# Optimization experiments

Measured on AMD Instinct MI355X. Metric: run time of the kernel, lower is better.

Reference implementation:

```python
import jax, jax.numpy as jnp
import numpy as np

NN_SIZE = 10  # k nearest neighbors (includes the point itself)
EPS = 1e-8


def batch_normals(points_nchw, nn_size):
    # points_nchw: (B, 3, N)
    x = jnp.transpose(points_nchw, (0, 2, 1))  # (B, N, 3)
    sq = jnp.sum(x * x, axis=-1)  # (B, N)
    # pairwise squared distances (B, N, N)
    d2 = sq[:, :, None] + sq[:, None, :] - 2.0 * jnp.einsum('bnd,bmd->bnm', x, x)
    _, idx = jax.lax.top_k(-d2, nn_size)  # (B, N, k) nearest-neighbor indices
    # irregular gather of neighborhoods: (B, N, k, 3)
    neigh = jax.vmap(lambda p, i: p[i])(x, idx)
    centered = neigh - jnp.mean(neigh, axis=2, keepdims=True)
    # local 3x3 covariance per point
    cov = jnp.einsum('bnki,bnkj->bnij', centered, centered) / nn_size
    _, vecs = jnp.linalg.eigh(cov)  # eigenvalues ascending
    normals = vecs[..., 0]  # eigenvector of smallest eigenvalue, (B, N, 3), unit norm
    return jnp.transpose(normals, (0, 2, 1))  # (B, 3, N)


def setup_inputs() -> dict:
    key = jax.random.key(0)
    k1, k2 = jax.random.split(key)
    pred = jax.random.normal(k1, (8, 3, 4096), dtype=jnp.float32)
    gt = jax.random.normal(k2, (8, 3, 4096), dtype=jnp.float32)
    return {"pred": pred, "gt": gt}


def reference(pred, gt):
    pn = batch_normals(pred, NN_SIZE)  # (B, 3, N)
    gn = batch_normals(gt, NN_SIZE)    # (B, 3, N)
    # cosine similarity along the channel (coordinate) dim
    dot = jnp.sum(pn * gn, axis=1)
    denom = jnp.sqrt(jnp.sum(pn * pn, axis=1)) * jnp.sqrt(jnp.sum(gn * gn, axis=1))
    cos = dot / jnp.maximum(denom, EPS)
    return jnp.mean(1.0 - jnp.abs(cos))
```

## Files before the change

### kernel.cpp

```cpp
#include <hip/hip_runtime.h>
#include <float.h>
#include <math.h>

#define BATCH 8
#define NPTS 4096
#define KNN 10
#define BN (BATCH * NPTS)
#define TPB 512
#define WAVES 8
#define QPB 128
#define HALFPTS 2048
#define SEGC (HALFPTS / WAVES)
#define GRIDX (NPTS / QPB)
#define KB_STRIDE (2 * KNN + 1)

__device__ inline float med3f(float x, float a, float b) {
    return __builtin_amdgcn_fmed3f(x, a, b);
}

#define INSERT(karr, key)                                              \
    do {                                                               \
        _Pragma("unroll")                                              \
        for (int _j = KNN - 1; _j >= 1; --_j)                          \
            karr[_j] = med3f((key), karr[_j - 1], karr[_j]);           \
        karr[0] = fminf((key), karr[0]);                               \
    } while (0)

__device__ inline void smallest_eigvec(float a00, float a01, float a02,
                                       float a11, float a12, float a22,
                                       float& vx, float& vy, float& vz) {
    float p1 = a01 * a01 + a02 * a02 + a12 * a12;
    float q = (a00 + a11 + a22) * (1.0f / 3.0f);
    float b00 = a00 - q, b11 = a11 - q, b22 = a22 - q;
    float p2 = b00 * b00 + b11 * b11 + b22 * b22 + 2.0f * p1;
    float p = sqrtf(p2 * (1.0f / 6.0f));
    if (p < 1e-20f) { vx = 1.0f; vy = 0.0f; vz = 0.0f; return; }
    float ip = 1.0f / p;
    float c00 = b00 * ip, c01 = a01 * ip, c02 = a02 * ip;
    float c11 = b11 * ip, c12 = a12 * ip, c22 = b22 * ip;
    float detB = c00 * (c11 * c22 - c12 * c12)
               - c01 * (c01 * c22 - c12 * c02)
               + c02 * (c01 * c12 - c11 * c02);
    float r = 0.5f * detB;
    r = fminf(1.0f, fmaxf(-1.0f, r));
    float phi = acosf(r) * (1.0f / 3.0f);
    float lmin = q + 2.0f * p * cosf(phi + 2.0943951023931953f);

    float m00 = a00 - lmin, m11 = a11 - lmin, m22 = a22 - lmin;
    float r0x = m00, r0y = a01, r0z = a02;
    float r1x = a01, r1y = m11, r1z = a12;
    float r2x = a02, r2y = a12, r2z = m22;
    float c0x = r0y * r1z - r0z * r1y, c0y = r0z * r1x - r0x * r1z, c0z = r0x * r1y - r0y * r1x;
    float c1x = r0y * r2z - r0z * r2y, c1y = r0z * r2x - r0x * r2z, c1z = r0x * r2y - r0y * r2x;
    float c2x = r1y * r2z - r1z * r2y, c2y = r1z * r2x - r1x * r2z, c2z = r1x * r2y - r1y * r2x;
    float n0 = c0x * c0x + c0y * c0y + c0z * c0z;
    float n1 = c1x * c1x + c1y * c1y + c1z * c1z;
    float n2 = c2x * c2x + c2y * c2y + c2z * c2z;
    float bx = c0x, by = c0y, bz = c0z, bnm = n0;
    if (n1 > bnm) { bx = c1x; by = c1y; bz = c1z; bnm = n1; }
    if (n2 > bnm) { bx = c2x; by = c2y; bz = c2z; bnm = n2; }
    if (bnm < 1e-30f) { vx = 1.0f; vy = 0.0f; vz = 0.0f; return; }
    float inv = rsqrtf(bnm);
    vx = bx * inv; vy = by * inv; vz = bz * inv;
}

#define STAGE(basep, pb)                                               \
    do {                                                               \
        for (int _i = tid; _i < HALFPTS; _i += TPB) {                  \
            float _x = (basep)[(pb) + _i];                             \
            float _y = (basep)[NPTS + (pb) + _i];                      \
            float _z = (basep)[2 * NPTS + (pb) + _i];                  \
            pts[_i] = make_float4(_x, _y, _z, fmaf(_x, _x, fmaf(_y, _y, _z * _z))); \
        }                                                              \
    } while (0)

#define SCAN_CLOUD(basep, ka, kb)                                      \
    do {                                                               \
        _Pragma("unroll")                                              \
        for (int _j = 0; _j < KNN; ++_j) { ka[_j] = FLT_MAX; kb[_j] = FLT_MAX; } \
        const float _a0x = -2.0f * (basep)[pt0];                       \
        const float _a0y = -2.0f * (basep)[NPTS + pt0];                \
        const float _a0z = -2.0f * (basep)[2 * NPTS + pt0];            \
        const float _a1x = -2.0f * (basep)[pt1];                       \
        const float _a1y = -2.0f * (basep)[NPTS + pt1];                \
        const float _a1z = -2.0f * (basep)[2 * NPTS + pt1];            \
        for (int _pass = 0; _pass < 2; ++_pass) {                      \
            const int _pb = _pass * HALFPTS;                           \
            STAGE(basep, _pb);                                         \
            __syncthreads();                                           \
            const unsigned _gb = (unsigned)(_pb + s0);                 \
            _Pragma("unroll 8")                                        \
            for (int _c = 0; _c < SEGC; ++_c) {                        \
                float4 _p = pts[s0 + _c];                              \
                float _d0 = fmaf(_p.z, _a0z, fmaf(_p.y, _a0y, fmaf(_p.x, _a0x, _p.w))); \
                float _d1 = fmaf(_p.z, _a1z, fmaf(_p.y, _a1y, fmaf(_p.x, _a1x, _p.w))); \
                unsigned _gi = _gb + (unsigned)_c;                     \
                float _k0 = __uint_as_float((__float_as_uint(_d0) & 0xFFFFF000u) | _gi); \
                float _k1 = __uint_as_float((__float_as_uint(_d1) & 0xFFFFF000u) | _gi); \
                INSERT(ka, _k0);                                       \
                INSERT(kb, _k1);                                       \
            }                                                          \
            __syncthreads();                                           \
        }                                                              \
          \
        for (int _half = WAVES / 2; _half >= 1; _half >>= 1) {         \
            if (w >= _half && w < 2 * _half) {                         \
                float* _dst = keybuf + ((w - _half) * 64 + lane) * KB_STRIDE; \
                _Pragma("unroll")                                      \
                for (int _j = 0; _j < KNN; ++_j) { _dst[_j] = ka[_j]; _dst[KNN + _j] = kb[_j]; } \
            }                                                          \
            __syncthreads();                                           \
            if (w < _half) {                                           \
                const float* _src = keybuf + (w * 64 + lane) * KB_STRIDE; \
                _Pragma("unroll")                                      \
                for (int _j = 0; _j < KNN; ++_j) {                     \
                    float _sa = _src[_j], _sb = _src[KNN + _j];        \
                    INSERT(ka, _sa);                                   \
                    INSERT(kb, _sb);                                   \
                }                                                      \
            }                                                          \
            __syncthreads();                                           \
        }                                                              \
    } while (0)

#define COMPUTE_NORMAL(karr, basep, vx, vy, vz)                        \
    do {                                                               \
        float _sx = 0.f, _sy = 0.f, _sz = 0.f;                         \
        float _sxx = 0.f, _sxy = 0.f, _sxz = 0.f;                      \
        float _syy = 0.f, _syz = 0.f, _szz = 0.f;                      \
        _Pragma("unroll")                                              \
        for (int _j = 0; _j < KNN; ++_j) {                             \
            int _idx = (int)(__float_as_uint(karr[_j]) & 0xFFFu);      \
            float _x = (basep)[_idx];                                  \
            float _y = (basep)[NPTS + _idx];                           \
            float _z = (basep)[2 * NPTS + _idx];                       \
            _sx += _x; _sy += _y; _sz += _z;                           \
            _sxx = fmaf(_x, _x, _sxx); _sxy = fmaf(_x, _y, _sxy); _sxz = fmaf(_x, _z, _sxz); \
            _syy = fmaf(_y, _y, _syy); _syz = fmaf(_y, _z, _syz); _szz = fmaf(_z, _z, _szz); \
        }                                                              \
        const float _iK = 1.0f / KNN;                                  \
        float _mx = _sx * _iK, _my = _sy * _iK, _mz = _sz * _iK;       \
        smallest_eigvec(_sxx * _iK - _mx * _mx, _sxy * _iK - _mx * _my, \
                        _sxz * _iK - _mx * _mz, _syy * _iK - _my * _my, \
                        _syz * _iK - _my * _mz, _szz * _iK - _mz * _mz, \
                        vx, vy, vz);                                   \
    } while (0)

__global__ void zero_out_kernel(float* __restrict__ out) {
    if (threadIdx.x == 0) out[0] = 0.0f;
}

__global__ __launch_bounds__(TPB, 2) void knn_normal_loss(
    const float* __restrict__ pred, const float* __restrict__ gt,
    float* __restrict__ out) {
    __shared__ float4 pts[HALFPTS];

    const int b = blockIdx.y;
    const float* __restrict__ baseP = pred + b * 3 * NPTS;
    const float* __restrict__ baseG = gt + b * 3 * NPTS;
    const int tid = threadIdx.x;
    const int lane = tid & 63;
    const int w = tid >> 6;
    const int s0 = w * SEGC;
    float* keybuf = (float*)pts;

    const int pt0 = blockIdx.x * QPB + lane;
    const int pt1 = pt0 + 64;

    float kP0[KNN], kP1[KNN];
    float kG0[KNN], kG1[KNN];

    SCAN_CLOUD(baseP, kP0, kP1);
    SCAN_CLOUD(baseG, kG0, kG1);

    if (w == 0) {
        float acc;
        {
            float pvx, pvy, pvz, gvx, gvy, gvz;
            COMPUTE_NORMAL(kP0, baseP, pvx, pvy, pvz);
            COMPUTE_NORMAL(kG0, baseG, gvx, gvy, gvz);
            float dot = pvx * gvx + pvy * gvy + pvz * gvz;
            float npn = sqrtf(pvx * pvx + pvy * pvy + pvz * pvz);
            float ngn = sqrtf(gvx * gvx + gvy * gvy + gvz * gvz);
            acc = 1.0f - fabsf(dot / fmaxf(npn * ngn, 1e-8f));
        }
        {
            float pvx, pvy, pvz, gvx, gvy, gvz;
            COMPUTE_NORMAL(kP1, baseP, pvx, pvy, pvz);
            COMPUTE_NORMAL(kG1, baseG, gvx, gvy, gvz);
            float dot = pvx * gvx + pvy * gvy + pvz * gvz;
            float npn = sqrtf(pvx * pvx + pvy * pvy + pvz * pvz);
            float ngn = sqrtf(gvx * gvx + gvy * gvy + gvz * gvz);
            acc += 1.0f - fabsf(dot / fmaxf(npn * ngn, 1e-8f));
        }
        for (int off = 32; off > 0; off >>= 1) acc += __shfl_down(acc, off);
        if (lane == 0) atomicAdd(out, acc * (1.0f / (float)BN));
    }
}

extern "C" void kernel_launch(void* const* d_in, const int* in_sizes, int n_in,
                              void* d_out, int out_size, void* d_ws, size_t ws_size,
                              hipStream_t stream) {
    const float* pred = (const float*)d_in[0];
    const float* gt = (const float*)d_in[1];
    float* out = (float*)d_out;

    zero_out_kernel<<<1, 64, 0, stream>>>(out);
    dim3 grid(GRIDX, BATCH);
    knn_normal_loss<<<grid, TPB, 0, stream>>>(pred, gt, out);
}
```

Baseline: 182.6 us.

## Use one query per thread with early-reject top-k insertion and more blocks

Each thread now tracks a single query point instead of two, halving queries per block and doubling the grid. Candidate distances are compared against the current k-th best before running the med3 insertion network, so most candidates skip the sorted insert. The scan loop is manually unrolled by eight LDS loads. In exchange, each staged point is reused by fewer queries, global staging traffic doubles, and the data-dependent branch can diverge within a wave.

```diff
diff --git a/kernel.cpp b/kernel.cpp
--- a/kernel.cpp
+++ b/kernel.cpp
@@ -8,11 +8,11 @@
 #define BN (BATCH * NPTS)
 #define TPB 512
 #define WAVES 8
-#define QPB 128
+#define QPB 64
 #define HALFPTS 2048
 #define SEGC (HALFPTS / WAVES)
 #define GRIDX (NPTS / QPB)
-#define KB_STRIDE (2 * KNN + 1)
+#define KB_STRIDE 11
 
 __device__ inline float med3f(float x, float a, float b) {
     return __builtin_amdgcn_fmed3f(x, a, b);
@@ -24,6 +24,13 @@
         for (int _j = KNN - 1; _j >= 1; --_j)                          \
             karr[_j] = med3f((key), karr[_j - 1], karr[_j]);           \
         karr[0] = fminf((key), karr[0]);                               \
+    } while (0)
+
+#define CAND(_p, _gi, karr)                                            \
+    do {                                                               \
+        float _d = fmaf((_p).z, a0z, fmaf((_p).y, a0y, fmaf((_p).x, a0x, (_p).w))); \
+        float _k = __uint_as_float((__float_as_uint(_d) & 0xFFFFF000u) | (_gi)); \
+        if (_k < karr[KNN - 1]) { INSERT(karr, _k); }                  \
     } while (0)
 
 __device__ inline void smallest_eigvec(float a00, float a01, float a02,
@@ -64,41 +71,41 @@
     vx = bx * inv; vy = by * inv; vz = bz * inv;
 }
 
-#define STAGE(basep, pb)                                               \
-    do {                                                               \
-        for (int _i = tid; _i < HALFPTS; _i += TPB) {                  \
-            float _x = (basep)[(pb) + _i];                             \
-            float _y = (basep)[NPTS + (pb) + _i];                      \
-            float _z = (basep)[2 * NPTS + (pb) + _i];                  \
-            pts[_i] = make_float4(_x, _y, _z, fmaf(_x, _x, fmaf(_y, _y, _z * _z))); \
-        }                                                              \
-    } while (0)
-
-#define SCAN_CLOUD(basep, ka, kb)                                      \
+#define SCAN_CLOUD(basep, karr)                                        \
     do {                                                               \
         _Pragma("unroll")                                              \
-        for (int _j = 0; _j < KNN; ++_j) { ka[_j] = FLT_MAX; kb[_j] = FLT_MAX; } \
-        const float _a0x = -2.0f * (basep)[pt0];                       \
-        const float _a0y = -2.0f * (basep)[NPTS + pt0];                \
-        const float _a0z = -2.0f * (basep)[2 * NPTS + pt0];            \
-        const float _a1x = -2.0f * (basep)[pt1];                       \
-        const float _a1y = -2.0f * (basep)[NPTS + pt1];                \
-        const float _a1z = -2.0f * (basep)[2 * NPTS + pt1];            \
+        for (int _j = 0; _j < KNN; ++_j) karr[_j] = FLT_MAX;           \
+        const float a0x = -2.0f * (basep)[pt];                         \
+        const float a0y = -2.0f * (basep)[NPTS + pt];                  \
+        const float a0z = -2.0f * (basep)[2 * NPTS + pt];              \
         for (int _pass = 0; _pass < 2; ++_pass) {                      \
             const int _pb = _pass * HALFPTS;                           \
-            STAGE(basep, _pb);                                         \
+            for (int _i = tid; _i < HALFPTS; _i += TPB) {              \
+                float _x = (basep)[_pb + _i];                          \
+                float _y = (basep)[NPTS + _pb + _i];                   \
+                float _z = (basep)[2 * NPTS + _pb + _i];               \
+                pts[_i] = make_float4(_x, _y, _z, fmaf(_x, _x, fmaf(_y, _y, _z * _z))); \
+            }                                                          \
             __syncthreads();                                           \
             const unsigned _gb = (unsigned)(_pb + s0);                 \
-            _Pragma("unroll 8")                                        \
-            for (int _c = 0; _c < SEGC; ++_c) {                        \
-                float4 _p = pts[s0 + _c];                              \
-                float _d0 = fmaf(_p.z, _a0z, fmaf(_p.y, _a0y, fmaf(_p.x, _a0x, _p.w))); \
-                float _d1 = fmaf(_p.z, _a1z, fmaf(_p.y, _a1y, fmaf(_p.x, _a1x, _p.w))); \
+            for (int _c = 0; _c < SEGC; _c += 8) {                     \
+                float4 _p0 = pts[s0 + _c + 0];                         \
+                float4 _p1 = pts[s0 + _c + 1];                         \
+                float4 _p2 = pts[s0 + _c + 2];                         \
+                float4 _p3 = pts[s0 + _c + 3];                         \
+                float4 _p4 = pts[s0 + _c + 4];                         \
+                float4 _p5 = pts[s0 + _c + 5];                         \
+                float4 _p6 = pts[s0 + _c + 6];                         \
+                float4 _p7 = pts[s0 + _c + 7];                         \
                 unsigned _gi = _gb + (unsigned)_c;                     \
-                float _k0 = __uint_as_float((__float_as_uint(_d0) & 0xFFFFF000u) | _gi); \
-                float _k1 = __uint_as_float((__float_as_uint(_d1) & 0xFFFFF000u) | _gi); \
-                INSERT(ka, _k0);                                       \
-                INSERT(kb, _k1);                                       \
+                CAND(_p0, _gi + 0, karr);                              \
+                CAND(_p1, _gi + 1, karr);                              \
+                CAND(_p2, _gi + 2, karr);                              \
+                CAND(_p3, _gi + 3, karr);                              \
+                CAND(_p4, _gi + 4, karr);                              \
+                CAND(_p5, _gi + 5, karr);                              \
+                CAND(_p6, _gi + 6, karr);                              \
+                CAND(_p7, _gi + 7, karr);                              \
             }                                                          \
             __syncthreads();                                           \
         }                                                              \
@@ -107,16 +114,15 @@
             if (w >= _half && w < 2 * _half) {                         \
                 float* _dst = keybuf + ((w - _half) * 64 + lane) * KB_STRIDE; \
                 _Pragma("unroll")                                      \
-                for (int _j = 0; _j < KNN; ++_j) { _dst[_j] = ka[_j]; _dst[KNN + _j] = kb[_j]; } \
+                for (int _j = 0; _j < KNN; ++_j) _dst[_j] = karr[_j];  \
             }                                                          \
             __syncthreads();                                           \
             if (w < _half) {                                           \
                 const float* _src = keybuf + (w * 64 + lane) * KB_STRIDE; \
                 _Pragma("unroll")                                      \
                 for (int _j = 0; _j < KNN; ++_j) {                     \
-                    float _sa = _src[_j], _sb = _src[KNN + _j];        \
-                    INSERT(ka, _sa);                                   \
-                    INSERT(kb, _sb);                                   \
+                    float _sk = _src[_j];                              \
+                    INSERT(karr, _sk);                                 \
                 }                                                      \
             }                                                          \
             __syncthreads();                                           \
@@ -164,35 +170,21 @@
     const int s0 = w * SEGC;
     float* keybuf = (float*)pts;
 
-    const int pt0 = blockIdx.x * QPB + lane;
-    const int pt1 = pt0 + 64;
-
-    float kP0[KNN], kP1[KNN];
-    float kG0[KNN], kG1[KNN];
-
-    SCAN_CLOUD(baseP, kP0, kP1);
-    SCAN_CLOUD(baseG, kG0, kG1);
+    const int pt = blockIdx.x * QPB + lane;
+
+    float kP[KNN], kG[KNN];
+
+    SCAN_CLOUD(baseP, kP);
+    SCAN_CLOUD(baseG, kG);
 
     if (w == 0) {
-        float acc;
-        {
-            float pvx, pvy, pvz, gvx, gvy, gvz;
-            COMPUTE_NORMAL(kP0, baseP, pvx, pvy, pvz);
-            COMPUTE_NORMAL(kG0, baseG, gvx, gvy, gvz);
-            float dot = pvx * gvx + pvy * gvy + pvz * gvz;
-            float npn = sqrtf(pvx * pvx + pvy * pvy + pvz * pvz);
-            float ngn = sqrtf(gvx * gvx + gvy * gvy + gvz * gvz);
-            acc = 1.0f - fabsf(dot / fmaxf(npn * ngn, 1e-8f));
-        }
-        {
-            float pvx, pvy, pvz, gvx, gvy, gvz;
-            COMPUTE_NORMAL(kP1, baseP, pvx, pvy, pvz);
-            COMPUTE_NORMAL(kG1, baseG, gvx, gvy, gvz);
-            float dot = pvx * gvx + pvy * gvy + pvz * gvz;
-            float npn = sqrtf(pvx * pvx + pvy * pvy + pvz * pvz);
-            float ngn = sqrtf(gvx * gvx + gvy * gvy + gvz * gvz);
-            acc += 1.0f - fabsf(dot / fmaxf(npn * ngn, 1e-8f));
-        }
+        float pvx, pvy, pvz, gvx, gvy, gvz;
+        COMPUTE_NORMAL(kP, baseP, pvx, pvy, pvz);
+        COMPUTE_NORMAL(kG, baseG, gvx, gvy, gvz);
+        float dot = pvx * gvx + pvy * gvy + pvz * gvz;
+        float npn = sqrtf(pvx * pvx + pvy * pvy + pvz * pvz);
+        float ngn = sqrtf(gvx * gvx + gvy * gvy + gvz * gvz);
+        float acc = 1.0f - fabsf(dot / fmaxf(npn * ngn, 1e-8f));
         for (int off = 32; off > 0; off >>= 1) acc += __shfl_down(acc, off);
         if (lane == 0) atomicAdd(out, acc * (1.0f / (float)BN));
     }
```

New measurement: 186.3 us. About the same (+2.0%).
